# Optimization experiments

Hardware: AMD Instinct MI355X
Metric: run time of the kernel (lower is better)

## Reference

```python
import jax, jax.numpy as jnp
import numpy as np
from jax import lax

B, T, D = 4, 4096, 1024
NEG_BIG = -1e30  # stand-in for -inf initial max-state; identical after clamp(min=-30)


def setup_inputs() -> dict:
    key = jax.random.key(0)
    ks = jax.random.split(key, 10)
    x = jax.random.normal(ks[0], (B, T, D), dtype=jnp.float32)
    time_mix_k = jax.random.uniform(ks[1], (D,), dtype=jnp.float32)
    time_mix_v = jax.random.uniform(ks[2], (D,), dtype=jnp.float32)
    time_mix_r = jax.random.uniform(ks[3], (D,), dtype=jnp.float32)
    s = 1.0 / np.sqrt(D)
    W_k = jax.random.normal(ks[4], (D, D), dtype=jnp.float32) * s
    W_v = jax.random.normal(ks[5], (D, D), dtype=jnp.float32) * s
    W_r = jax.random.normal(ks[6], (D, D), dtype=jnp.float32) * s
    W_o = jax.random.normal(ks[7], (D, D), dtype=jnp.float32) * s
    time_decay = -(jax.random.uniform(ks[8], (D,), dtype=jnp.float32) + 0.5)
    time_first = jax.random.normal(ks[9], (D,), dtype=jnp.float32) * 0.1
    return {"x": x, "time_mix_k": time_mix_k, "time_mix_v": time_mix_v,
            "time_mix_r": time_mix_r, "W_k": W_k, "W_v": W_v, "W_r": W_r,
            "W_o": W_o, "time_decay": time_decay, "time_first": time_first}


def _wkv_scan(k, v, w, u):
    # k, v: [B, T, D]; w, u: [D]. Numerically-stable max-subtract WKV scan.
    b, t, d = k.shape
    p0 = jnp.full((b, d), NEG_BIG, dtype=k.dtype)  # running max exponent
    q0 = jnp.zeros((b, d), dtype=k.dtype)          # rescaled numerator state

    def step(carry, kv_t):
        p, q = carry
        k_t, v_t = kv_t
        new_p = jnp.maximum(p, u + k_t)
        scale_old = jnp.exp(jnp.maximum(p - new_p, -30.0))
        scale_cur = jnp.exp(jnp.maximum(u + k_t - new_p, -30.0))
        wkv = (scale_old * q + scale_cur * v_t) / (scale_old + scale_cur + 1e-9)
        new_p2 = jnp.maximum(p + w, k_t)
        scale_prev = jnp.exp(jnp.maximum(p + w - new_p2, -30.0))
        scale_new = jnp.exp(jnp.maximum(k_t - new_p2, -30.0))
        q2 = scale_prev * q + scale_new * v_t
        return (new_p2, q2), wkv

    kT = jnp.swapaxes(k, 0, 1)  # [T, B, D]
    vT = jnp.swapaxes(v, 0, 1)
    _, wkv = lax.scan(step, (p0, q0), (kT, vT))
    return jnp.swapaxes(wkv, 0, 1)  # [B, T, D]


def reference(x, time_mix_k, time_mix_v, time_mix_r, W_k, W_v, W_r, W_o,
              time_decay, time_first):
    # token shift: x_prev[t] = x[t-1], zeros at t=0
    x_prev = jnp.pad(x[:, :-1, :], ((0, 0), (1, 0), (0, 0)))
    xk = x * time_mix_k + x_prev * (1.0 - time_mix_k)
    xv = x * time_mix_v + x_prev * (1.0 - time_mix_v)
    xr = x * time_mix_r + x_prev * (1.0 - time_mix_r)
    # torch nn.Linear (no bias): y = x @ W.T
    k = jnp.einsum('btd,ed->bte', xk, W_k)
    v = jnp.einsum('btd,ed->bte', xv, W_v)
    r = jax.nn.sigmoid(jnp.einsum('btd,ed->bte', xr, W_r))
    wkv = _wkv_scan(k, v, time_decay, time_first)
    y = r * wkv
    return jnp.einsum('btd,ed->bte', y, W_o)
```

## Files before the change

### kernel.cpp

```cpp
#include <hip/hip_runtime.h>
#include <stdint.h>

#define D_DIM 1024
#define T_DIM 4096
#define B_DIM 4
#define M_DIM (B_DIM * T_DIM)
#define NCH 64
#define CHL 64

typedef short bf16x8 __attribute__((ext_vector_type(8)));
typedef float f32x4 __attribute__((ext_vector_type(4)));

__device__ __forceinline__ ushort f2bf(float f) {
    union { float f; uint32_t u; } x; x.f = f;
    uint32_t r = x.u + 0x7fffu + ((x.u >> 16) & 1u);
    return (ushort)(r >> 16);
}
__device__ __forceinline__ float bf2f(ushort u) {
    union { uint32_t u; float f; } x; x.u = (uint32_t)u << 16; return x.f;
}

__device__ __forceinline__ void gload16(const ushort* g, ushort* l) {
    __builtin_amdgcn_global_load_lds(
        (const __attribute__((address_space(1))) void*)g,
        (__attribute__((address_space(3))) void*)l, 16, 0, 0);
}

__global__ void convw(const float* __restrict__ w0, const float* __restrict__ w1,
                      const float* __restrict__ w2, const float* __restrict__ w3,
                      ushort* __restrict__ out) {
    int i = blockIdx.x * 256 + threadIdx.x;
    int sel = i >> 18;
    const float* src = sel == 0 ? w0 : sel == 1 ? w1 : sel == 2 ? w2 : w3;
    int off = (i & 0x3ffff) << 2;
    float4 f = *(const float4*)(src + off);
    ushort4 o; o.x = f2bf(f.x); o.y = f2bf(f.y); o.z = f2bf(f.z); o.w = f2bf(f.w);
    *(ushort4*)(out + (size_t)i * 4) = o;
}

__global__ void mixz(const float* __restrict__ x, const float* __restrict__ tm,
                     ushort* __restrict__ o) {
    size_t gid = (size_t)blockIdx.x * 256 + threadIdx.x;
    size_t e = gid * 4;
    int d = (int)(e & (D_DIM - 1));
    int t = (int)((e >> 10) & (T_DIM - 1));
    float4 xc = *(const float4*)(x + e);
    float4 xp = make_float4(0.f, 0.f, 0.f, 0.f);
    if (t > 0) xp = *(const float4*)(x + e - D_DIM);
    float4 m = *(const float4*)(tm + d);
    ushort4 r;
    r.x = f2bf(xc.x * m.x + xp.x * (1.f - m.x));
    r.y = f2bf(xc.y * m.y + xp.y * (1.f - m.y));
    r.z = f2bf(xc.z * m.z + xp.z * (1.f - m.z));
    r.w = f2bf(xc.w * m.w + xp.w * (1.f - m.w));
    *(ushort4*)(o + e) = r;
}

template <int OUTF32>
__global__ void __launch_bounds__(256)
gemm_bt(const ushort* __restrict__ A, const ushort* __restrict__ Bw,
        void* __restrict__ Cv) {
    constexpr int K = 1024, N = 1024;
    __shared__ ushort As[128 * 32];
    __shared__ ushort Bs[128 * 32];
    const int tid = threadIdx.x;
    const int wid = tid >> 6, lane = tid & 63;
    const int wr = wid >> 1, wc = wid & 1;

    const ushort* Ab = A + (size_t)blockIdx.y * 128 * K;
    const ushort* Bb = Bw + (size_t)blockIdx.x * 128 * K;
    const ushort* ga = Ab + (size_t)(tid >> 2) * K + ((tid & 3) << 3);
    const ushort* gb = Bb + (size_t)(tid >> 2) * K + ((tid & 3) << 3);
    ushort* lA0 = &As[wid * 512];
    ushort* lA1 = &As[2048 + wid * 512];
    ushort* lB0 = &Bs[wid * 512];
    ushort* lB1 = &Bs[2048 + wid * 512];
    const size_t rstep = (size_t)64 * K;

    f32x4 acc[4][4] = {};
    const int frow = lane & 15;
    const int kgrp = (lane >> 4) << 3;

    for (int kt = 0; kt < K; kt += 32) {
        __syncthreads();
        gload16(ga + kt, lA0);
        gload16(ga + kt + rstep, lA1);
        gload16(gb + kt, lB0);
        gload16(gb + kt + rstep, lB1);
        __syncthreads();
        bf16x8 af[4], bfr[4];
#pragma unroll
        for (int m = 0; m < 4; ++m)
            af[m] = *(const bf16x8*)&As[(wr * 64 + m * 16 + frow) * 32 + kgrp];
#pragma unroll
        for (int n = 0; n < 4; ++n)
            bfr[n] = *(const bf16x8*)&Bs[(wc * 64 + n * 16 + frow) * 32 + kgrp];
#pragma unroll
        for (int m = 0; m < 4; ++m)
#pragma unroll
            for (int n = 0; n < 4; ++n)
                acc[m][n] = __builtin_amdgcn_mfma_f32_16x16x32_bf16(
                    af[m], bfr[n], acc[m][n], 0, 0, 0);
    }

    const int rsub = (lane >> 4) << 2;
    const int col = blockIdx.x * 128 + wc * 64 + frow;
    const int row0 = blockIdx.y * 128 + wr * 64 + rsub;
#pragma unroll
    for (int m = 0; m < 4; ++m)
#pragma unroll
        for (int n = 0; n < 4; ++n)
#pragma unroll
            for (int r = 0; r < 4; ++r) {
                size_t idx = (size_t)(row0 + m * 16 + r) * N + col + n * 16;
                if (OUTF32)
                    ((float*)Cv)[idx] = acc[m][n][r];
                else
                    ((ushort*)Cv)[idx] = f2bf(acc[m][n][r]);
            }
}

__global__ void wkv_passA(const ushort* __restrict__ k, const ushort* __restrict__ v,
                          const float* __restrict__ w_, float* __restrict__ m_arr,
                          float* __restrict__ s_arr) {
    int gid = blockIdx.x * 256 + threadIdx.x;
    int d = gid & 1023;
    int b = (gid >> 10) & 3;
    int c = gid >> 12;
    float w = w_[d];
    size_t base = ((size_t)(b * T_DIM + c * CHL)) * D_DIM + d;
    float m = -1e30f, s = 0.f;
#pragma unroll 4
    for (int i = 0; i < CHL; ++i) {
        float kk = bf2f(k[base + (size_t)i * D_DIM]);
        float vv = bf2f(v[base + (size_t)i * D_DIM]);
        float e = kk + (float)(CHL - 1 - i) * w;
        float nm = fmaxf(m, e);
        s = s * __expf(fmaxf(m - nm, -30.f)) + __expf(fmaxf(e - nm, -30.f)) * vv;
        m = nm;
    }
    m_arr[gid] = m;
    s_arr[gid] = s;
}

__global__ void wkv_passB(const float* __restrict__ m_arr, const float* __restrict__ s_arr,
                          const float* __restrict__ w_, float* __restrict__ pin,
                          float* __restrict__ qin) {
    int gid = blockIdx.x * 256 + threadIdx.x;
    int d = gid & 1023;
    int b = gid >> 10;
    float w = w_[d];
    float Lw = (float)CHL * w;
    float p = -1e30f, q = 0.f;
    for (int c = 0; c < NCH; ++c) {
        int idx = ((c * B_DIM + b) << 10) | d;
        pin[idx] = p; qin[idx] = q;
        float mc = m_arr[idx], sc = s_arr[idx];
        float pn = fmaxf(p + Lw, mc);
        q = __expf(fmaxf(p + Lw - pn, -30.f)) * q +
            __expf(fmaxf(mc - pn, -30.f)) * sc;
        p = pn;
    }
}

__global__ void wkv_passC(const ushort* __restrict__ k, const ushort* __restrict__ v,
                          const ushort* __restrict__ r, const float* __restrict__ w_,
                          const float* __restrict__ u_, const float* __restrict__ pin,
                          const float* __restrict__ qin, ushort* __restrict__ y) {
    int gid = blockIdx.x * 256 + threadIdx.x;
    int d = gid & 1023;
    int b = (gid >> 10) & 3;
    int c = gid >> 12;
    float w = w_[d], u = u_[d];
    float p = pin[gid], q = qin[gid];
    size_t base = ((size_t)(b * T_DIM + c * CHL)) * D_DIM + d;
#pragma unroll 4
    for (int i = 0; i < CHL; ++i) {
        float kk = bf2f(k[base]), vv = bf2f(v[base]), rr = bf2f(r[base]);
        float uk = u + kk;
        float np = fmaxf(p, uk);
        float so = __expf(fmaxf(p - np, -30.f));
        float sc = __expf(fmaxf(uk - np, -30.f));
        float wkv = (so * q + sc * vv) / (so + sc + 1e-9f);
        float np2 = fmaxf(p + w, kk);
        float sp = __expf(fmaxf(p + w - np2, -30.f));
        float sn = __expf(fmaxf(kk - np2, -30.f));
        q = sp * q + sn * vv;
        p = np2;
        float sig = 1.f / (1.f + __expf(-rr));
        y[base] = f2bf(sig * wkv);
        base += D_DIM;
    }
}

extern "C" void kernel_launch(void* const* d_in, const int* in_sizes, int n_in,
                              void* d_out, int out_size, void* d_ws, size_t ws_size,
                              hipStream_t stream) {
    (void)in_sizes; (void)n_in; (void)out_size;
    const float* x  = (const float*)d_in[0];
    const float* mk = (const float*)d_in[1];
    const float* mv = (const float*)d_in[2];
    const float* mr = (const float*)d_in[3];
    const float* Wk = (const float*)d_in[4];
    const float* Wv = (const float*)d_in[5];
    const float* Wr = (const float*)d_in[6];
    const float* Wo = (const float*)d_in[7];
    const float* td = (const float*)d_in[8];
    const float* tf = (const float*)d_in[9];

    const size_t MD = (size_t)M_DIM * D_DIM;
    const size_t DD = (size_t)D_DIM * D_DIM;
    const size_t CHN = (size_t)B_DIM * D_DIM * NCH;

    ushort* wcat = (ushort*)d_ws;
    ushort* kbuf = wcat + 4 * DD;
    ushort* vbuf = kbuf + MD;
    ushort* rbuf = vbuf + MD;
    ushort* xbuf = rbuf + MD;
    float* m_arr = (float*)(xbuf + MD);
    float* s_arr = m_arr + CHN;
    float* pin   = s_arr + CHN;
    float* qin   = pin + CHN;
    size_t need = (size_t)((char*)(qin + CHN) - (char*)d_ws);
    if (ws_size < need) return;

    dim3 ggrid(8, 128, 1);

    convw<<<4096, 256, 0, stream>>>(Wk, Wv, Wr, Wo, wcat);

    mixz<<<16384, 256, 0, stream>>>(x, mk, xbuf);
    gemm_bt<0><<<ggrid, 256, 0, stream>>>(xbuf, wcat, kbuf);
    mixz<<<16384, 256, 0, stream>>>(x, mv, xbuf);
    gemm_bt<0><<<ggrid, 256, 0, stream>>>(xbuf, wcat + DD, vbuf);
    mixz<<<16384, 256, 0, stream>>>(x, mr, xbuf);
    gemm_bt<0><<<ggrid, 256, 0, stream>>>(xbuf, wcat + 2 * DD, rbuf);

    wkv_passA<<<1024, 256, 0, stream>>>(kbuf, vbuf, td, m_arr, s_arr);
    wkv_passB<<<16, 256, 0, stream>>>(m_arr, s_arr, td, pin, qin);
    wkv_passC<<<1024, 256, 0, stream>>>(kbuf, vbuf, rbuf, td, tf, pin, qin, xbuf);

    gemm_bt<1><<<ggrid, 256, 0, stream>>>(xbuf, wcat + 3 * DD, d_out);
}
```

Measured before the change: 471.2 us.

## Fuse token-mix kernels, batch k/v/r GEMMs, vectorize WKV passes, stage GEMM stores

Replaces the three token-mix launches with a single kernel that reads x once and writes all three mixed inputs. The k/v/r projections become one GEMM launch over blockIdx.z, with a remapped block index intended to improve L2 reuse. The bf16 GEMM epilogue now stages each tile through LDS so global stores are coalesced 16-byte writes. The WKV chunk passes A and C handle four channels per thread with vector loads, which cuts their launch sizes from 1024 to 256 blocks. The fused path needs a larger workspace and falls back to the old schedule when the workspace is too small.

```diff
diff --git a/kernel.cpp b/kernel.cpp
--- a/kernel.cpp
+++ b/kernel.cpp
@@ -7,6 +7,8 @@
 #define M_DIM (B_DIM * T_DIM)
 #define NCH 64
 #define CHL 64
+#define GEMM_N 1024
+#define GEMM_K 1024
 
 typedef short bf16x8 __attribute__((ext_vector_type(8)));
 typedef float f32x4 __attribute__((ext_vector_type(4)));
@@ -56,19 +58,60 @@
     *(ushort4*)(o + e) = r;
 }
 
+__global__ void mixall(const float* __restrict__ x,
+                       const float* __restrict__ mk, const float* __restrict__ mv,
+                       const float* __restrict__ mr,
+                       ushort* __restrict__ xk, ushort* __restrict__ xv,
+                       ushort* __restrict__ xr) {
+    size_t gid = (size_t)blockIdx.x * 256 + threadIdx.x;
+    size_t e = gid * 4;
+    int d = (int)(e & (D_DIM - 1));
+    int t = (int)((e >> 10) & (T_DIM - 1));
+    float4 xc = *(const float4*)(x + e);
+    float4 xp = make_float4(0.f, 0.f, 0.f, 0.f);
+    if (t > 0) xp = *(const float4*)(x + e - D_DIM);
+    float4 a = *(const float4*)(mk + d);
+    float4 b = *(const float4*)(mv + d);
+    float4 c = *(const float4*)(mr + d);
+    ushort4 ok, ov, orr;
+    ok.x = f2bf(xc.x * a.x + xp.x * (1.f - a.x));
+    ok.y = f2bf(xc.y * a.y + xp.y * (1.f - a.y));
+    ok.z = f2bf(xc.z * a.z + xp.z * (1.f - a.z));
+    ok.w = f2bf(xc.w * a.w + xp.w * (1.f - a.w));
+    ov.x = f2bf(xc.x * b.x + xp.x * (1.f - b.x));
+    ov.y = f2bf(xc.y * b.y + xp.y * (1.f - b.y));
+    ov.z = f2bf(xc.z * b.z + xp.z * (1.f - b.z));
+    ov.w = f2bf(xc.w * b.w + xp.w * (1.f - b.w));
+    orr.x = f2bf(xc.x * c.x + xp.x * (1.f - c.x));
+    orr.y = f2bf(xc.y * c.y + xp.y * (1.f - c.y));
+    orr.z = f2bf(xc.z * c.z + xp.z * (1.f - c.z));
+    orr.w = f2bf(xc.w * c.w + xp.w * (1.f - c.w));
+    *(ushort4*)(xk + e) = ok;
+    *(ushort4*)(xv + e) = ov;
+    *(ushort4*)(xr + e) = orr;
+}
+
 template <int OUTF32>
 __global__ void __launch_bounds__(256)
-gemm_bt(const ushort* __restrict__ A, const ushort* __restrict__ Bw,
-        void* __restrict__ Cv) {
-    constexpr int K = 1024, N = 1024;
+gemm_bt(const ushort* __restrict__ A0, const ushort* __restrict__ B0,
+        void* __restrict__ Cv, size_t sA, size_t sB, size_t sC) {
+    constexpr int K = GEMM_K, N = GEMM_N;
     __shared__ ushort As[128 * 32];
     __shared__ ushort Bs[128 * 32];
+    const int z = blockIdx.z;
+    const ushort* A = A0 + (size_t)z * sA;
+    const ushort* Bw = B0 + (size_t)z * sB;
+
+    const int id = blockIdx.y * 8 + blockIdx.x;
+    const int L = (id & 7) * 128 + (id >> 3);
+    const int bx = L & 7, by = L >> 3;
+
     const int tid = threadIdx.x;
     const int wid = tid >> 6, lane = tid & 63;
     const int wr = wid >> 1, wc = wid & 1;
 
-    const ushort* Ab = A + (size_t)blockIdx.y * 128 * K;
-    const ushort* Bb = Bw + (size_t)blockIdx.x * 128 * K;
+    const ushort* Ab = A + (size_t)by * 128 * K;
+    const ushort* Bb = Bw + (size_t)bx * 128 * K;
     const ushort* ga = Ab + (size_t)(tid >> 2) * K + ((tid & 3) << 3);
     const ushort* gb = Bb + (size_t)(tid >> 2) * K + ((tid & 3) << 3);
     ushort* lA0 = &As[wid * 512];
@@ -104,43 +147,76 @@
     }
 
     const int rsub = (lane >> 4) << 2;
-    const int col = blockIdx.x * 128 + wc * 64 + frow;
-    const int row0 = blockIdx.y * 128 + wr * 64 + rsub;
-#pragma unroll
-    for (int m = 0; m < 4; ++m)
-#pragma unroll
-        for (int n = 0; n < 4; ++n)
-#pragma unroll
-            for (int r = 0; r < 4; ++r) {
-                size_t idx = (size_t)(row0 + m * 16 + r) * N + col + n * 16;
-                if (OUTF32)
-                    ((float*)Cv)[idx] = acc[m][n][r];
-                else
-                    ((ushort*)Cv)[idx] = f2bf(acc[m][n][r]);
+    if (OUTF32) {
+        float* C = (float*)Cv + (size_t)z * sC;
+        const int col = bx * 128 + wc * 64 + frow;
+        const int row0 = by * 128 + wr * 64 + rsub;
+#pragma unroll
+        for (int m = 0; m < 4; ++m)
+#pragma unroll
+            for (int n = 0; n < 4; ++n)
+#pragma unroll
+                for (int r = 0; r < 4; ++r)
+                    C[(size_t)(row0 + m * 16 + r) * N + col + n * 16] = acc[m][n][r];
+    } else {
+        ushort* C = (ushort*)Cv + (size_t)z * sC;
+        ushort* Cs = As;
+        const int gRow0 = by * 128, gCol0 = bx * 128;
+#pragma unroll
+        for (int ch = 0; ch < 4; ++ch) {
+            __syncthreads();
+            if ((ch >> 1) == wr) {
+                const int mb = (ch & 1) << 1;
+#pragma unroll
+                for (int mm = 0; mm < 2; ++mm)
+#pragma unroll
+                    for (int n = 0; n < 4; ++n)
+#pragma unroll
+                        for (int r = 0; r < 4; ++r) {
+                            int lr = ((mb + mm) & 1) * 16 + rsub + r;
+                            int lc = wc * 64 + n * 16 + frow;
+                            Cs[lr * 128 + lc] = f2bf(acc[mb + mm][n][r]);
+                        }
             }
-}
-
-__global__ void wkv_passA(const ushort* __restrict__ k, const ushort* __restrict__ v,
-                          const float* __restrict__ w_, float* __restrict__ m_arr,
-                          float* __restrict__ s_arr) {
+            __syncthreads();
+            const int lr1 = tid >> 4, lc1 = (tid & 15) << 3;
+            size_t g1 = (size_t)(gRow0 + ch * 32 + lr1) * N + gCol0 + lc1;
+            size_t g2 = (size_t)(gRow0 + ch * 32 + 16 + lr1) * N + gCol0 + lc1;
+            *(bf16x8*)(C + g1) = *(const bf16x8*)&Cs[tid << 3];
+            *(bf16x8*)(C + g2) = *(const bf16x8*)&Cs[2048 + (tid << 3)];
+        }
+    }
+}
+
+__global__ void wkv_passA4(const ushort* __restrict__ k, const ushort* __restrict__ v,
+                           const float* __restrict__ w_, float* __restrict__ m_arr,
+                           float* __restrict__ s_arr) {
     int gid = blockIdx.x * 256 + threadIdx.x;
-    int d = gid & 1023;
-    int b = (gid >> 10) & 3;
-    int c = gid >> 12;
-    float w = w_[d];
-    size_t base = ((size_t)(b * T_DIM + c * CHL)) * D_DIM + d;
-    float m = -1e30f, s = 0.f;
-#pragma unroll 4
+    int d4 = gid & 255;
+    int b = (gid >> 8) & 3;
+    int c = gid >> 10;
+    float4 w4 = *(const float4*)(w_ + d4 * 4);
+    size_t base = ((size_t)(b * T_DIM + c * CHL)) * D_DIM + d4 * 4;
+    float m0 = -1e30f, m1 = -1e30f, m2 = -1e30f, m3 = -1e30f;
+    float s0 = 0.f, s1 = 0.f, s2 = 0.f, s3 = 0.f;
+#pragma unroll 2
     for (int i = 0; i < CHL; ++i) {
-        float kk = bf2f(k[base + (size_t)i * D_DIM]);
-        float vv = bf2f(v[base + (size_t)i * D_DIM]);
-        float e = kk + (float)(CHL - 1 - i) * w;
-        float nm = fmaxf(m, e);
-        s = s * __expf(fmaxf(m - nm, -30.f)) + __expf(fmaxf(e - nm, -30.f)) * vv;
-        m = nm;
-    }
-    m_arr[gid] = m;
-    s_arr[gid] = s;
+        ushort4 k4 = *(const ushort4*)(k + base + (size_t)i * D_DIM);
+        ushort4 v4 = *(const ushort4*)(v + base + (size_t)i * D_DIM);
+        float cw = (float)(CHL - 1 - i);
+        float e0 = bf2f(k4.x) + cw * w4.x, e1 = bf2f(k4.y) + cw * w4.y;
+        float e2 = bf2f(k4.z) + cw * w4.z, e3 = bf2f(k4.w) + cw * w4.w;
+        float n0 = fmaxf(m0, e0), n1 = fmaxf(m1, e1);
+        float n2 = fmaxf(m2, e2), n3 = fmaxf(m3, e3);
+        s0 = s0 * __expf(fmaxf(m0 - n0, -30.f)) + __expf(fmaxf(e0 - n0, -30.f)) * bf2f(v4.x);
+        s1 = s1 * __expf(fmaxf(m1 - n1, -30.f)) + __expf(fmaxf(e1 - n1, -30.f)) * bf2f(v4.y);
+        s2 = s2 * __expf(fmaxf(m2 - n2, -30.f)) + __expf(fmaxf(e2 - n2, -30.f)) * bf2f(v4.z);
+        s3 = s3 * __expf(fmaxf(m3 - n3, -30.f)) + __expf(fmaxf(e3 - n3, -30.f)) * bf2f(v4.w);
+        m0 = n0; m1 = n1; m2 = n2; m3 = n3;
+    }
+    int idx = ((c * B_DIM + b) << 10) + d4 * 4;
+    *(float4*)(m_arr + idx) = make_float4(m0, m1, m2, m3);
+    *(float4*)(s_arr + idx) = make_float4(s0, s1, s2, s3);
 }
 
 __global__ void wkv_passB(const float* __restrict__ m_arr, const float* __restrict__ s_arr,
@@ -163,32 +239,50 @@
     }
 }
 
-__global__ void wkv_passC(const ushort* __restrict__ k, const ushort* __restrict__ v,
-                          const ushort* __restrict__ r, const float* __restrict__ w_,
-                          const float* __restrict__ u_, const float* __restrict__ pin,
-                          const float* __restrict__ qin, ushort* __restrict__ y) {
+__global__ void wkv_passC4(const ushort* __restrict__ k, const ushort* __restrict__ v,
+                           const ushort* __restrict__ r, const float* __restrict__ w_,
+                           const float* __restrict__ u_, const float* __restrict__ pin,
+                           const float* __restrict__ qin, ushort* __restrict__ y) {
     int gid = blockIdx.x * 256 + threadIdx.x;
-    int d = gid & 1023;
-    int b = (gid >> 10) & 3;
-    int c = gid >> 12;
-    float w = w_[d], u = u_[d];
-    float p = pin[gid], q = qin[gid];
-    size_t base = ((size_t)(b * T_DIM + c * CHL)) * D_DIM + d;
-#pragma unroll 4
+    int d4 = gid & 255;
+    int b = (gid >> 8) & 3;
+    int c = gid >> 10;
+    float4 w4 = *(const float4*)(w_ + d4 * 4);
+    float4 u4 = *(const float4*)(u_ + d4 * 4);
+    int sidx = ((c * B_DIM + b) << 10) + d4 * 4;
+    float4 p4 = *(const float4*)(pin + sidx);
+    float4 q4 = *(const float4*)(qin + sidx);
+    float p0 = p4.x, p1 = p4.y, p2 = p4.z, p3 = p4.w;
+    float q0 = q4.x, q1 = q4.y, q2 = q4.z, q3 = q4.w;
+    size_t base = ((size_t)(b * T_DIM + c * CHL)) * D_DIM + d4 * 4;
+#pragma unroll 2
     for (int i = 0; i < CHL; ++i) {
-        float kk = bf2f(k[base]), vv = bf2f(v[base]), rr = bf2f(r[base]);
-        float uk = u + kk;
-        float np = fmaxf(p, uk);
-        float so = __expf(fmaxf(p - np, -30.f));
-        float sc = __expf(fmaxf(uk - np, -30.f));
-        float wkv = (so * q + sc * vv) / (so + sc + 1e-9f);
-        float np2 = fmaxf(p + w, kk);
-        float sp = __expf(fmaxf(p + w - np2, -30.f));
-        float sn = __expf(fmaxf(kk - np2, -30.f));
-        q = sp * q + sn * vv;
-        p = np2;
-        float sig = 1.f / (1.f + __expf(-rr));
-        y[base] = f2bf(sig * wkv);
+        ushort4 k4 = *(const ushort4*)(k + base);
+        ushort4 v4 = *(const ushort4*)(v + base);
+        ushort4 r4 = *(const ushort4*)(r + base);
+        ushort4 o;
+#define WKV_CH(P, Q, KK, VV, RR, W, U, OUT)                                   \
+        {                                                                     \
+            float kk = bf2f(KK), vv = bf2f(VV), rr = bf2f(RR);                \
+            float uk = (U) + kk;                                              \
+            float np = fmaxf(P, uk);                                          \
+            float so = __expf(fmaxf(P - np, -30.f));                          \
+            float sc = __expf(fmaxf(uk - np, -30.f));                         \
+            float wkv = (so * Q + sc * vv) / (so + sc + 1e-9f);               \
+            float np2 = fmaxf(P + (W), kk);                                   \
+            float sp = __expf(fmaxf(P + (W) - np2, -30.f));                   \
+            float sn = __expf(fmaxf(kk - np2, -30.f));                        \
+            Q = sp * Q + sn * vv;                                             \
+            P = np2;                                                          \
+            float sig = 1.f / (1.f + __expf(-rr));                            \
+            OUT = f2bf(sig * wkv);                                            \
+        }
+        WKV_CH(p0, q0, k4.x, v4.x, r4.x, w4.x, u4.x, o.x)
+        WKV_CH(p1, q1, k4.y, v4.y, r4.y, w4.y, u4.y, o.y)
+        WKV_CH(p2, q2, k4.z, v4.z, r4.z, w4.z, u4.z, o.z)
+        WKV_CH(p3, q3, k4.w, v4.w, r4.w, w4.w, u4.w, o.w)
+#undef WKV_CH
+        *(ushort4*)(y + base) = o;
         base += D_DIM;
     }
 }
@@ -212,32 +306,52 @@
     const size_t DD = (size_t)D_DIM * D_DIM;
     const size_t CHN = (size_t)B_DIM * D_DIM * NCH;
 
-    ushort* wcat = (ushort*)d_ws;
-    ushort* kbuf = wcat + 4 * DD;
-    ushort* vbuf = kbuf + MD;
-    ushort* rbuf = vbuf + MD;
-    ushort* xbuf = rbuf + MD;
-    float* m_arr = (float*)(xbuf + MD);
-    float* s_arr = m_arr + CHN;
-    float* pin   = s_arr + CHN;
-    float* qin   = pin + CHN;
-    size_t need = (size_t)((char*)(qin + CHN) - (char*)d_ws);
-    if (ws_size < need) return;
-
-    dim3 ggrid(8, 128, 1);
-
-    convw<<<4096, 256, 0, stream>>>(Wk, Wv, Wr, Wo, wcat);
-
-    mixz<<<16384, 256, 0, stream>>>(x, mk, xbuf);
-    gemm_bt<0><<<ggrid, 256, 0, stream>>>(xbuf, wcat, kbuf);
-    mixz<<<16384, 256, 0, stream>>>(x, mv, xbuf);
-    gemm_bt<0><<<ggrid, 256, 0, stream>>>(xbuf, wcat + DD, vbuf);
-    mixz<<<16384, 256, 0, stream>>>(x, mr, xbuf);
-    gemm_bt<0><<<ggrid, 256, 0, stream>>>(xbuf, wcat + 2 * DD, rbuf);
-
-    wkv_passA<<<1024, 256, 0, stream>>>(kbuf, vbuf, td, m_arr, s_arr);
-    wkv_passB<<<16, 256, 0, stream>>>(m_arr, s_arr, td, pin, qin);
-    wkv_passC<<<1024, 256, 0, stream>>>(kbuf, vbuf, rbuf, td, tf, pin, qin, xbuf);
-
-    gemm_bt<1><<<ggrid, 256, 0, stream>>>(xbuf, wcat + 3 * DD, d_out);
-}
+    size_t need_big = (4 * DD + 6 * MD) * 2 + 4 * CHN * 4;
+    size_t need_small = (4 * DD + 4 * MD) * 2 + 4 * CHN * 4;
+    if (ws_size < need_small) return;
+
+    dim3 g1(8, 128, 1), g3(8, 128, 3);
+
+    if (ws_size >= need_big) {
+        ushort* wcat = (ushort*)d_ws;
+        ushort* xcat = wcat + 4 * DD;
+        ushort* kvr  = xcat + 3 * MD;
+        float* m_arr = (float*)(kvr + 3 * MD);
+        float* s_arr = m_arr + CHN;
+        float* pin   = s_arr + CHN;
+        float* qin   = pin + CHN;
+        ushort* ybuf = xcat;
+
+        convw<<<4096, 256, 0, stream>>>(Wk, Wv, Wr, Wo, wcat);
+        mixall<<<16384, 256, 0, stream>>>(x, mk, mv, mr,
+                                          xcat, xcat + MD, xcat + 2 * MD);
+        gemm_bt<0><<<g3, 256, 0, stream>>>(xcat, wcat, kvr, MD, DD, MD);
+        wkv_passA4<<<256, 256, 0, stream>>>(kvr, kvr + MD, td, m_arr, s_arr);
+        wkv_passB<<<16, 256, 0, stream>>>(m_arr, s_arr, td, pin, qin);
+        wkv_passC4<<<256, 256, 0, stream>>>(kvr, kvr + MD, kvr + 2 * MD,
+                                            td, tf, pin, qin, ybuf);
+        gemm_bt<1><<<g1, 256, 0, stream>>>(ybuf, wcat + 3 * DD, d_out, 0, 0, 0);
+    } else {
+        ushort* wcat = (ushort*)d_ws;
+        ushort* kbuf = wcat + 4 * DD;
+        ushort* vbuf = kbuf + MD;
+        ushort* rbuf = vbuf + MD;
+        ushort* xbuf = rbuf + MD;
+        float* m_arr = (float*)(xbuf + MD);
+        float* s_arr = m_arr + CHN;
+        float* pin   = s_arr + CHN;
+        float* qin   = pin + CHN;
+
+        convw<<<4096, 256, 0, stream>>>(Wk, Wv, Wr, Wo, wcat);
+        mixz<<<16384, 256, 0, stream>>>(x, mk, xbuf);
+        gemm_bt<0><<<g1, 256, 0, stream>>>(xbuf, wcat, kbuf, 0, 0, 0);
+        mixz<<<16384, 256, 0, stream>>>(x, mv, xbuf);
+        gemm_bt<0><<<g1, 256, 0, stream>>>(xbuf, wcat + DD, vbuf, 0, 0, 0);
+        mixz<<<16384, 256, 0, stream>>>(x, mr, xbuf);
+        gemm_bt<0><<<g1, 256, 0, stream>>>(xbuf, wcat + 2 * DD, rbuf, 0, 0, 0);
+        wkv_passA4<<<256, 256, 0, stream>>>(kbuf, vbuf, td, m_arr, s_arr);
+        wkv_passB<<<16, 256, 0, stream>>>(m_arr, s_arr, td, pin, qin);
+        wkv_passC4<<<256, 256, 0, stream>>>(kbuf, vbuf, rbuf, td, tf, pin, qin, xbuf);
+        gemm_bt<1><<<g1, 256, 0, stream>>>(xbuf, wcat + 3 * DD, d_out, 0, 0, 0);
+    }
+}
```

Measured after the change: 445.4 us. 1.06x faster.
